# Optimization experiments

Measured on AMD Instinct MI355X. Metric: run time of the kernel, lower is better.

The kernel has to match this reference:

```python
import jax, jax.numpy as jnp
import numpy as np

N_NODES = 100000
N_EDGES = 1000000
IN_DIM = 128
HID1 = 64
HID2 = 64
OUT_DIM = 1
NUM_GRAPHS = 2048


def setup_inputs() -> dict:
    key = jax.random.key(0)
    ks = jax.random.split(key, 12)
    x = jax.random.normal(ks[0], (N_NODES, IN_DIM), dtype=jnp.float32)
    edge_index = jax.random.randint(ks[1], (2, N_EDGES), 0, N_NODES, dtype=jnp.int64)
    batch = jnp.sort(jax.random.randint(ks[2], (N_NODES,), 0, NUM_GRAPHS, dtype=jnp.int64))
    s1 = 1.0 / np.sqrt(IN_DIM)
    s2 = 1.0 / np.sqrt(HID1)
    s3 = 1.0 / np.sqrt(HID2)
    return {
        "x": x,
        "edge_index": edge_index,
        "batch": batch,
        "W1": jax.random.normal(ks[3], (IN_DIM, HID1), dtype=jnp.float32) * s1,
        "b1": jnp.zeros((HID1,), dtype=jnp.float32),
        "W2": jax.random.normal(ks[4], (HID1, HID2), dtype=jnp.float32) * s2,
        "b2": jnp.zeros((HID2,), dtype=jnp.float32),
        "attn_w": jax.random.normal(ks[5], (HID2, 1), dtype=jnp.float32) * s3,
        "attn_b": jnp.zeros((1,), dtype=jnp.float32),
        "mask_w": jax.random.normal(ks[6], (HID2, 1), dtype=jnp.float32) * s3,
        "mask_b": jnp.zeros((1,), dtype=jnp.float32),
        "out_w": jax.random.normal(ks[7], (HID2, OUT_DIM), dtype=jnp.float32) * s3,
        "out_b": jnp.zeros((OUT_DIM,), dtype=jnp.float32),
    }


def reference(x, edge_index, batch, W1, b1, W2, b2, attn_w, attn_b, mask_w, mask_b, out_w, out_b):
    n = x.shape[0]
    # GCNConv (PyG default): add self-loops, symmetric normalization
    loop = jnp.arange(n, dtype=edge_index.dtype)
    row = jnp.concatenate([edge_index[0], loop])  # source nodes
    col = jnp.concatenate([edge_index[1], loop])  # target nodes
    deg = jax.ops.segment_sum(jnp.ones_like(col, dtype=x.dtype), col, num_segments=n)
    dinv = jnp.where(deg > 0, jax.lax.rsqrt(jnp.maximum(deg, 1e-12)), 0.0)
    norm = dinv[row] * dinv[col]  # [E+N]

    def conv(h, W, b):
        h = h @ W                              # [N, out]
        m = h[row] * norm[:, None]             # gather + scale  [E+N, out]
        return jax.ops.segment_sum(m, col, num_segments=n) + b

    h = jax.nn.relu(conv(x, W1, b1))
    h = jax.nn.relu(conv(h, W2, b2))
    # AttentionPooling: (attn score * sigmoid mask)-weighted scatter-sum per graph
    scores = (h @ attn_w + attn_b) * jax.nn.sigmoid(h @ mask_w + mask_b)  # [N,1]
    pooled = jax.ops.segment_sum(h * scores, batch, num_segments=NUM_GRAPHS)  # [G, HID2]
    return pooled @ out_w + out_b
```

## Files before the change

### kernel.cpp

```cpp
#include <hip/hip_runtime.h>
#include <math.h>


#define NB 64
#define SEG 16
#define CAPS 80
#define SLOTS (SEG * CAPS)
#define BIN_BLOCKS 256

__global__ __launch_bounds__(256) void gemm_bin_kernel(
    const float* __restrict__ X, const float* __restrict__ W,
    float* __restrict__ P, int N, int K,
    const int* __restrict__ row, const int* __restrict__ col,
    int* __restrict__ bcnt, int* __restrict__ gbuf, int E,
    float* __restrict__ out, const float* __restrict__ out_b, int G) {
    __shared__ float Wl[32 * 64];
    __shared__ float xs[128 * 33];

    if (blockIdx.x < BIN_BLOCKS) {
        int seg = blockIdx.x & (SEG - 1);
        int t = blockIdx.x * 256 + threadIdx.x;
        if (t < G) out[t] = out_b[0];
        for (int e = t; e < E; e += BIN_BLOCKS * 256) {
            int c = col[e];
            int b = c >> 6;
            int pos = atomicAdd(&bcnt[(b * SEG + seg) * 16], 1);
            if (pos < CAPS) gbuf[b * SLOTS + seg * CAPS + pos] = row[e] | ((c & 63) << 17);
        }
        return;
    }

    const int tid = threadIdx.x;
    const int cg = tid & 3;
    const int ng = tid >> 2;
    const int node0 = (blockIdx.x - BIN_BLOCKS) * 128;

    float acc[2][16];
#pragma unroll
    for (int r = 0; r < 2; r++)
#pragma unroll
        for (int j = 0; j < 16; j++) acc[r][j] = 0.0f;

    for (int k0 = 0; k0 < K; k0 += 32) {
        const float4* Wg = (const float4*)(W + (size_t)k0 * 64);
#pragma unroll
        for (int f = tid; f < 512; f += 256) ((float4*)Wl)[f] = Wg[f];
        {
            int rrow = tid >> 1;
            int q0 = (tid & 1) * 16;
            int node = node0 + rrow;
            const float* Xr = X + (size_t)node * K + k0 + q0;
            float* xd = &xs[rrow * 33 + q0];
#pragma unroll
            for (int q = 0; q < 4; q++) {
                float4 v = make_float4(0.f, 0.f, 0.f, 0.f);
                if (node < N) v = *(const float4*)(Xr + 4 * q);
                xd[4 * q + 0] = v.x;
                xd[4 * q + 1] = v.y;
                xd[4 * q + 2] = v.z;
                xd[4 * q + 3] = v.w;
            }
        }
        __syncthreads();
#pragma unroll
        for (int kk = 0; kk < 32; kk++) {
            float xv0 = xs[(ng * 2 + 0) * 33 + kk];
            float xv1 = xs[(ng * 2 + 1) * 33 + kk];
            const float* wr = &Wl[kk * 64 + cg * 4];
            float4 w0 = *(const float4*)(wr + 0);
            float4 w1 = *(const float4*)(wr + 16);
            float4 w2 = *(const float4*)(wr + 32);
            float4 w3 = *(const float4*)(wr + 48);
#pragma unroll
            for (int r = 0; r < 2; r++) {
                float xv = r ? xv1 : xv0;
                acc[r][0]  = fmaf(xv, w0.x, acc[r][0]);
                acc[r][1]  = fmaf(xv, w0.y, acc[r][1]);
                acc[r][2]  = fmaf(xv, w0.z, acc[r][2]);
                acc[r][3]  = fmaf(xv, w0.w, acc[r][3]);
                acc[r][4]  = fmaf(xv, w1.x, acc[r][4]);
                acc[r][5]  = fmaf(xv, w1.y, acc[r][5]);
                acc[r][6]  = fmaf(xv, w1.z, acc[r][6]);
                acc[r][7]  = fmaf(xv, w1.w, acc[r][7]);
                acc[r][8]  = fmaf(xv, w2.x, acc[r][8]);
                acc[r][9]  = fmaf(xv, w2.y, acc[r][9]);
                acc[r][10] = fmaf(xv, w2.z, acc[r][10]);
                acc[r][11] = fmaf(xv, w2.w, acc[r][11]);
                acc[r][12] = fmaf(xv, w3.x, acc[r][12]);
                acc[r][13] = fmaf(xv, w3.y, acc[r][13]);
                acc[r][14] = fmaf(xv, w3.z, acc[r][14]);
                acc[r][15] = fmaf(xv, w3.w, acc[r][15]);
            }
        }
        __syncthreads();
    }

#pragma unroll
    for (int r = 0; r < 2; r++) {
        int node = node0 + ng * 2 + r;
        if (node < N) {
            float* dst = P + (size_t)node * 64 + cg * 4;
#pragma unroll
            for (int m = 0; m < 4; m++) {
                float4 v = make_float4(acc[r][4 * m + 0], acc[r][4 * m + 1],
                                       acc[r][4 * m + 2], acc[r][4 * m + 3]);
                *(float4*)(dst + 16 * m) = v;
            }
        }
    }
}

__global__ __launch_bounds__(256) void sort_kernel(
    const int* __restrict__ bcnt, const int* __restrict__ gbuf,
    int* __restrict__ csr, int* __restrict__ startcnt,
    float* __restrict__ dinv, int N) {
    __shared__ int scnt[SEG], segoff[SEG], s_tot;
    __shared__ int ebuf[SLOTS];
    __shared__ int lcnt[NB], lcur[NB];
    const int tid = threadIdx.x;
    const int b = blockIdx.x;
    const int base = b * SLOTS;

    if (tid < SEG) {
        int c = bcnt[(b * SEG + tid) * 16];
        scnt[tid] = c < CAPS ? c : CAPS;
    }
    if (tid < NB) lcnt[tid] = 0;
    __syncthreads();
    if (tid == 0) {
        int o = 0;
        for (int s = 0; s < SEG; s++) { segoff[s] = o; o += scnt[s]; }
        s_tot = o;
    }
    __syncthreads();
    for (int idx = tid; idx < SLOTS; idx += 256) {
        int seg = idx / CAPS;
        int j = idx - seg * CAPS;
        if (j < scnt[seg]) {
            int w = gbuf[base + idx];
            ebuf[segoff[seg] + j] = w;
            atomicAdd(&lcnt[(w >> 17) & 63], 1);
        }
    }
    __syncthreads();
    if (tid < NB) {
        int cntv = lcnt[tid];
        int rnd = (cntv + 3) & ~3;
        int val = rnd;
#pragma unroll
        for (int off = 1; off < 64; off <<= 1) {
            int n = __shfl_up(val, off, 64);
            if (tid >= off) val += n;
        }
        int st = val - rnd;
        lcur[tid] = st;
        int v = b * NB + tid;
        if (v < N) {
            dinv[v] = rsqrtf(1.0f + (float)cntv);
            int cc = cntv < 127 ? cntv : 127;
            startcnt[v] = ((base + st) << 7) | cc;
        }
    }
    __syncthreads();
    int tot = s_tot;
    for (int idx = tid; idx < tot; idx += 256) {
        int w = ebuf[idx];
        int vl = (w >> 17) & 63;
        int pp = atomicAdd(&lcur[vl], 1);
        csr[base + pp] = w & 131071;
    }
}

__global__ __launch_bounds__(256) void gather_gemm_kernel(
    const float* __restrict__ P, const int* __restrict__ csr,
    const int* __restrict__ startcnt, const float* __restrict__ dinv,
    const float* __restrict__ b1, const float* __restrict__ W2,
    float* __restrict__ Q, int N) {
    __shared__ float hs[64 * 65];
    __shared__ float Wl[64 * 64];
    const int tid = threadIdx.x;
    const int v0 = blockIdx.x * 64;
    const int vend = (v0 + 64 < N) ? v0 + 64 : N;
    const int p = tid & 15;
    const int p4 = p * 4;

    for (int f = tid; f < 1024; f += 256)
        ((float4*)Wl)[f] = ((const float4*)W2)[f];

    const float4 bb = ((const float4*)b1)[p];
    for (int v = v0 + (tid >> 4); v < vend; v += 16) {
        int pack = startcnt[v];
        int st = pack >> 7;
        int c = pack & 127;
        float dv = dinv[v];
        float4 a0 = *(const float4*)(P + (size_t)v * 64 + p4);
        float4 acc = make_float4(a0.x * dv, a0.y * dv, a0.z * dv, a0.w * dv);
        for (int i = 0; i < c; i += 8) {
            int4 ua = *(const int4*)(csr + st + i);
            int4 ub = *(const int4*)(csr + st + i + 4);
            float du0 = dinv[ua.x], du1 = dinv[ua.y], du2 = dinv[ua.z], du3 = dinv[ua.w];
            float du4 = dinv[ub.x], du5 = dinv[ub.y], du6 = dinv[ub.z], du7 = dinv[ub.w];
            float4 m0 = *(const float4*)(P + (size_t)ua.x * 64 + p4);
            float4 m1 = *(const float4*)(P + (size_t)ua.y * 64 + p4);
            float4 m2 = *(const float4*)(P + (size_t)ua.z * 64 + p4);
            float4 m3 = *(const float4*)(P + (size_t)ua.w * 64 + p4);
            float4 m4 = *(const float4*)(P + (size_t)ub.x * 64 + p4);
            float4 m5 = *(const float4*)(P + (size_t)ub.y * 64 + p4);
            float4 m6 = *(const float4*)(P + (size_t)ub.z * 64 + p4);
            float4 m7 = *(const float4*)(P + (size_t)ub.w * 64 + p4);
            acc.x = fmaf(m0.x, du0, acc.x); acc.y = fmaf(m0.y, du0, acc.y);
            acc.z = fmaf(m0.z, du0, acc.z); acc.w = fmaf(m0.w, du0, acc.w);
            if (i + 1 < c) { acc.x = fmaf(m1.x, du1, acc.x); acc.y = fmaf(m1.y, du1, acc.y);
                             acc.z = fmaf(m1.z, du1, acc.z); acc.w = fmaf(m1.w, du1, acc.w); }
            if (i + 2 < c) { acc.x = fmaf(m2.x, du2, acc.x); acc.y = fmaf(m2.y, du2, acc.y);
                             acc.z = fmaf(m2.z, du2, acc.z); acc.w = fmaf(m2.w, du2, acc.w); }
            if (i + 3 < c) { acc.x = fmaf(m3.x, du3, acc.x); acc.y = fmaf(m3.y, du3, acc.y);
                             acc.z = fmaf(m3.z, du3, acc.z); acc.w = fmaf(m3.w, du3, acc.w); }
            if (i + 4 < c) { acc.x = fmaf(m4.x, du4, acc.x); acc.y = fmaf(m4.y, du4, acc.y);
                             acc.z = fmaf(m4.z, du4, acc.z); acc.w = fmaf(m4.w, du4, acc.w); }
            if (i + 5 < c) { acc.x = fmaf(m5.x, du5, acc.x); acc.y = fmaf(m5.y, du5, acc.y);
                             acc.z = fmaf(m5.z, du5, acc.z); acc.w = fmaf(m5.w, du5, acc.w); }
            if (i + 6 < c) { acc.x = fmaf(m6.x, du6, acc.x); acc.y = fmaf(m6.y, du6, acc.y);
                             acc.z = fmaf(m6.z, du6, acc.z); acc.w = fmaf(m6.w, du6, acc.w); }
            if (i + 7 < c) { acc.x = fmaf(m7.x, du7, acc.x); acc.y = fmaf(m7.y, du7, acc.y);
                             acc.z = fmaf(m7.z, du7, acc.z); acc.w = fmaf(m7.w, du7, acc.w); }
        }
        float* hd = &hs[(v - v0) * 65 + p4];
        hd[0] = fmaxf(fmaf(acc.x, dv, bb.x), 0.f);
        hd[1] = fmaxf(fmaf(acc.y, dv, bb.y), 0.f);
        hd[2] = fmaxf(fmaf(acc.z, dv, bb.z), 0.f);
        hd[3] = fmaxf(fmaf(acc.w, dv, bb.w), 0.f);
    }
    __syncthreads();

    const int cg = tid & 3;
    const int n0 = tid >> 2;
    float acc[16];
#pragma unroll
    for (int j = 0; j < 16; j++) acc[j] = 0.0f;
    for (int kk = 0; kk < 64; kk++) {
        float xv = hs[n0 * 65 + kk];
        const float* wr = &Wl[kk * 64 + cg * 4];
        float4 w0 = *(const float4*)(wr + 0);
        float4 w1 = *(const float4*)(wr + 16);
        float4 w2 = *(const float4*)(wr + 32);
        float4 w3 = *(const float4*)(wr + 48);
        acc[0]  = fmaf(xv, w0.x, acc[0]);
        acc[1]  = fmaf(xv, w0.y, acc[1]);
        acc[2]  = fmaf(xv, w0.z, acc[2]);
        acc[3]  = fmaf(xv, w0.w, acc[3]);
        acc[4]  = fmaf(xv, w1.x, acc[4]);
        acc[5]  = fmaf(xv, w1.y, acc[5]);
        acc[6]  = fmaf(xv, w1.z, acc[6]);
        acc[7]  = fmaf(xv, w1.w, acc[7]);
        acc[8]  = fmaf(xv, w2.x, acc[8]);
        acc[9]  = fmaf(xv, w2.y, acc[9]);
        acc[10] = fmaf(xv, w2.z, acc[10]);
        acc[11] = fmaf(xv, w2.w, acc[11]);
        acc[12] = fmaf(xv, w3.x, acc[12]);
        acc[13] = fmaf(xv, w3.y, acc[13]);
        acc[14] = fmaf(xv, w3.z, acc[14]);
        acc[15] = fmaf(xv, w3.w, acc[15]);
    }
    int node = v0 + n0;
    if (node < N) {
        float d = dinv[node];
        float* dst = Q + (size_t)node * 64 + cg * 4;
        for (int m = 0; m < 4; m++) {
            float4 v = make_float4(acc[4 * m + 0] * d, acc[4 * m + 1] * d,
                                   acc[4 * m + 2] * d, acc[4 * m + 3] * d);
            *(float4*)(dst + 16 * m) = v;
        }
    }
}

#define GP_NODES 64
__global__ __launch_bounds__(256) void gather_pool_kernel(
    const float* __restrict__ Q, const int* __restrict__ csr,
    const int* __restrict__ startcnt, const float* __restrict__ dinv,
    const float* __restrict__ bias, const int* __restrict__ batch,
    const float* __restrict__ attn_w, const float* __restrict__ attn_b,
    const float* __restrict__ mask_w, const float* __restrict__ mask_b,
    const float* __restrict__ out_w, float* __restrict__ out, int N) {
    __shared__ float pacc[2048];
    __shared__ int s_gmin, s_span;
    const int tid = threadIdx.x;
    const int v0 = blockIdx.x * GP_NODES;
    const int vend = (v0 + GP_NODES < N) ? v0 + GP_NODES : N;
    if (tid == 0) {
        int gmin = batch[v0];
        s_gmin = gmin;
        s_span = batch[vend - 1] - gmin + 1;
    }
    __syncthreads();
    const int gmin = s_gmin, span = s_span;
    for (int i = tid; i < span; i += 256) pacc[i] = 0.f;
    __syncthreads();

    const int p = tid & 15;
    const int p4 = p * 4;
    const float4 wa = ((const float4*)attn_w)[p];
    const float4 wm = ((const float4*)mask_w)[p];
    const float4 wo = ((const float4*)out_w)[p];
    const float4 bb = ((const float4*)bias)[p];
    const float ab = attn_b[0], mb = mask_b[0];

    for (int v = v0 + (tid >> 4); v < vend; v += 16) {
        int pack = startcnt[v];
        int st = pack >> 7;
        int c = pack & 127;
        float dv = dinv[v];
        float4 acc = *(const float4*)(Q + (size_t)v * 64 + p4);
        for (int i = 0; i < c; i += 8) {
            int4 ua = *(const int4*)(csr + st + i);
            int4 ub = *(const int4*)(csr + st + i + 4);
            float4 m0 = *(const float4*)(Q + (size_t)ua.x * 64 + p4);
            float4 m1 = *(const float4*)(Q + (size_t)ua.y * 64 + p4);
            float4 m2 = *(const float4*)(Q + (size_t)ua.z * 64 + p4);
            float4 m3 = *(const float4*)(Q + (size_t)ua.w * 64 + p4);
            float4 m4 = *(const float4*)(Q + (size_t)ub.x * 64 + p4);
            float4 m5 = *(const float4*)(Q + (size_t)ub.y * 64 + p4);
            float4 m6 = *(const float4*)(Q + (size_t)ub.z * 64 + p4);
            float4 m7 = *(const float4*)(Q + (size_t)ub.w * 64 + p4);
            acc.x += m0.x; acc.y += m0.y; acc.z += m0.z; acc.w += m0.w;
            if (i + 1 < c) { acc.x += m1.x; acc.y += m1.y; acc.z += m1.z; acc.w += m1.w; }
            if (i + 2 < c) { acc.x += m2.x; acc.y += m2.y; acc.z += m2.z; acc.w += m2.w; }
            if (i + 3 < c) { acc.x += m3.x; acc.y += m3.y; acc.z += m3.z; acc.w += m3.w; }
            if (i + 4 < c) { acc.x += m4.x; acc.y += m4.y; acc.z += m4.z; acc.w += m4.w; }
            if (i + 5 < c) { acc.x += m5.x; acc.y += m5.y; acc.z += m5.z; acc.w += m5.w; }
            if (i + 6 < c) { acc.x += m6.x; acc.y += m6.y; acc.z += m6.z; acc.w += m6.w; }
            if (i + 7 < c) { acc.x += m7.x; acc.y += m7.y; acc.z += m7.z; acc.w += m7.w; }
        }
        float hx = fmaxf(fmaf(acc.x, dv, bb.x), 0.f);
        float hy = fmaxf(fmaf(acc.y, dv, bb.y), 0.f);
        float hz = fmaxf(fmaf(acc.z, dv, bb.z), 0.f);
        float hw = fmaxf(fmaf(acc.w, dv, bb.w), 0.f);
        float pa = hx * wa.x + hy * wa.y + hz * wa.z + hw * wa.w;
        float pm = hx * wm.x + hy * wm.y + hz * wm.z + hw * wm.w;
        float po = hx * wo.x + hy * wo.y + hz * wo.z + hw * wo.w;
#pragma unroll
        for (int off = 1; off < 16; off <<= 1) {
            pa += __shfl_xor(pa, off, 64);
            pm += __shfl_xor(pm, off, 64);
            po += __shfl_xor(po, off, 64);
        }
        if (p == 0) {
            float cc = (pa + ab) * (1.0f / (1.0f + expf(-(pm + mb)))) * po;
            atomicAdd(&pacc[batch[v] - gmin], cc);
        }
    }
    __syncthreads();
    for (int i = tid; i < span; i += 256) {
        float val = pacc[i];
        if (val != 0.f) atomicAdd(&out[gmin + i], val);
    }
}

extern "C" void kernel_launch(void* const* d_in, const int* in_sizes, int n_in,
                              void* d_out, int out_size, void* d_ws, size_t ws_size,
                              hipStream_t stream) {
    const float* x      = (const float*)d_in[0];
    const int*   edge   = (const int*)d_in[1];
    const int*   batch  = (const int*)d_in[2];
    const float* W1     = (const float*)d_in[3];
    const float* b1     = (const float*)d_in[4];
    const float* W2     = (const float*)d_in[5];
    const float* b2     = (const float*)d_in[6];
    const float* attn_w = (const float*)d_in[7];
    const float* attn_b = (const float*)d_in[8];
    const float* mask_w = (const float*)d_in[9];
    const float* mask_b = (const float*)d_in[10];
    const float* out_w  = (const float*)d_in[11];
    const float* out_b  = (const float*)d_in[12];
    float* out = (float*)d_out;

    const int N  = in_sizes[2];
    const int E  = in_sizes[1] / 2;
    const int K1 = in_sizes[0] / N;
    const int H  = in_sizes[4];
    const int G  = out_size;
    const int* row = edge;
    const int* col = edge + E;

    const int NBUCK = (N + NB - 1) / NB;

    char* ws = (char*)d_ws;
    auto align256 = [](size_t s) { return (s + 255) / 256 * 256; };
    int*   bcnt     = (int*)ws;   ws += align256((size_t)NBUCK * SEG * 16 * 4);
    int*   gbuf     = (int*)ws;   ws += align256((size_t)NBUCK * SLOTS * 4);
    int*   csr      = (int*)ws;   ws += align256((size_t)NBUCK * SLOTS * 4);
    int*   startcnt = (int*)ws;   ws += align256((size_t)N * 4);
    float* dinv     = (float*)ws; ws += align256((size_t)N * 4);
    float* P        = (float*)ws; ws += align256((size_t)N * H * 4);
    float* Q        = (float*)ws;

    const int gblocks = (N + 127) / 128;

    hipMemsetAsync(bcnt, 0, (size_t)NBUCK * SEG * 16 * 4, stream);
    hipMemsetAsync(csr, 0, (size_t)NBUCK * SLOTS * 4, stream);

    gemm_bin_kernel<<<BIN_BLOCKS + gblocks, 256, 0, stream>>>(
        x, W1, P, N, K1, row, col, bcnt, gbuf, E, out, out_b, G);

    sort_kernel<<<NBUCK, 256, 0, stream>>>(bcnt, gbuf, csr, startcnt, dinv, N);

    gather_gemm_kernel<<<NBUCK, 256, 0, stream>>>(
        P, csr, startcnt, dinv, b1, W2, Q, N);

    gather_pool_kernel<<<NBUCK, 256, 0, stream>>>(
        Q, csr, startcnt, dinv, b2, batch, attn_w, attn_b, mask_w, mask_b, out_w, out, N);
}
```

Baseline: 275.9 us.

## Move first GEMM from bin kernel into sort kernel, widen binning grid

Splits edge binning into a standalone kernel with four times as many blocks, and co-schedules the X@W1 GEMM blocks with the per-bucket sort blocks in one launch that shares a union shared-memory buffer. The aim is for the atomic-heavy binning to get full occupancy on its own, while the compute-bound GEMM overlaps the latency-bound sort. The cost is that the GEMM no longer overlaps the binning, and the wider grid raises atomic contention on the bucket counters.

```diff
diff --git a/kernel.cpp b/kernel.cpp
--- a/kernel.cpp
+++ b/kernel.cpp
@@ -6,34 +6,97 @@
 #define SEG 16
 #define CAPS 80
 #define SLOTS (SEG * CAPS)
-#define BIN_BLOCKS 256
-
-__global__ __launch_bounds__(256) void gemm_bin_kernel(
-    const float* __restrict__ X, const float* __restrict__ W,
-    float* __restrict__ P, int N, int K,
+#define BIN_BLOCKS 1024
+
+__global__ __launch_bounds__(256) void bin_kernel(
     const int* __restrict__ row, const int* __restrict__ col,
     int* __restrict__ bcnt, int* __restrict__ gbuf, int E,
     float* __restrict__ out, const float* __restrict__ out_b, int G) {
-    __shared__ float Wl[32 * 64];
-    __shared__ float xs[128 * 33];
-
-    if (blockIdx.x < BIN_BLOCKS) {
-        int seg = blockIdx.x & (SEG - 1);
-        int t = blockIdx.x * 256 + threadIdx.x;
-        if (t < G) out[t] = out_b[0];
-        for (int e = t; e < E; e += BIN_BLOCKS * 256) {
-            int c = col[e];
-            int b = c >> 6;
-            int pos = atomicAdd(&bcnt[(b * SEG + seg) * 16], 1);
-            if (pos < CAPS) gbuf[b * SLOTS + seg * CAPS + pos] = row[e] | ((c & 63) << 17);
+    int seg = blockIdx.x & (SEG - 1);
+    int t = blockIdx.x * 256 + threadIdx.x;
+    if (t < G) out[t] = out_b[0];
+    for (int e = t; e < E; e += BIN_BLOCKS * 256) {
+        int c = col[e];
+        int b = c >> 6;
+        int pos = atomicAdd(&bcnt[(b * SEG + seg) * 16], 1);
+        if (pos < CAPS) gbuf[b * SLOTS + seg * CAPS + pos] = row[e] | ((c & 63) << 17);
+    }
+}
+
+__global__ __launch_bounds__(256) void sort_gemm_kernel(
+    const int* __restrict__ bcnt, const int* __restrict__ gbuf,
+    int* __restrict__ csr, int* __restrict__ startcnt, float* __restrict__ dinv,
+    const float* __restrict__ X, const float* __restrict__ W,
+    float* __restrict__ P, int N, int K, int nbuck) {
+    __shared__ __align__(16) char smem[25088];
+    const int tid = threadIdx.x;
+
+    if ((int)blockIdx.x < nbuck) {
+        int* scnt   = (int*)smem;
+        int* segoff = scnt + SEG;
+        int* s_tot  = segoff + SEG;
+        int* lcnt   = s_tot + 1;
+        int* lcur   = lcnt + NB;
+        int* ebuf   = lcur + NB;
+        const int b = blockIdx.x;
+        const int base = b * SLOTS;
+
+        if (tid < SEG) {
+            int c = bcnt[(b * SEG + tid) * 16];
+            scnt[tid] = c < CAPS ? c : CAPS;
+        }
+        if (tid < NB) lcnt[tid] = 0;
+        __syncthreads();
+        if (tid == 0) {
+            int o = 0;
+            for (int s = 0; s < SEG; s++) { segoff[s] = o; o += scnt[s]; }
+            *s_tot = o;
+        }
+        __syncthreads();
+        for (int idx = tid; idx < SLOTS; idx += 256) {
+            int seg = idx / CAPS;
+            int j = idx - seg * CAPS;
+            if (j < scnt[seg]) {
+                int w = gbuf[base + idx];
+                ebuf[segoff[seg] + j] = w;
+                atomicAdd(&lcnt[(w >> 17) & 63], 1);
+            }
+        }
+        __syncthreads();
+        if (tid < NB) {
+            int cntv = lcnt[tid];
+            int rnd = (cntv + 3) & ~3;
+            int val = rnd;
+#pragma unroll
+            for (int off = 1; off < 64; off <<= 1) {
+                int n = __shfl_up(val, off, 64);
+                if (tid >= off) val += n;
+            }
+            int st = val - rnd;
+            lcur[tid] = st;
+            int v = b * NB + tid;
+            if (v < N) {
+                dinv[v] = rsqrtf(1.0f + (float)cntv);
+                int cc = cntv < 127 ? cntv : 127;
+                startcnt[v] = ((base + st) << 7) | cc;
+            }
+        }
+        __syncthreads();
+        int tot = *s_tot;
+        for (int idx = tid; idx < tot; idx += 256) {
+            int w = ebuf[idx];
+            int vl = (w >> 17) & 63;
+            int pp = atomicAdd(&lcur[vl], 1);
+            csr[base + pp] = w & 131071;
         }
         return;
     }
 
-    const int tid = threadIdx.x;
+    float* Wl = (float*)smem;
+    float* xs = Wl + 32 * 64;
     const int cg = tid & 3;
     const int ng = tid >> 2;
-    const int node0 = (blockIdx.x - BIN_BLOCKS) * 128;
+    const int node0 = (blockIdx.x - nbuck) * 128;
 
     float acc[2][16];
 #pragma unroll
@@ -107,67 +170,6 @@
                 *(float4*)(dst + 16 * m) = v;
             }
         }
-    }
-}
-
-__global__ __launch_bounds__(256) void sort_kernel(
-    const int* __restrict__ bcnt, const int* __restrict__ gbuf,
-    int* __restrict__ csr, int* __restrict__ startcnt,
-    float* __restrict__ dinv, int N) {
-    __shared__ int scnt[SEG], segoff[SEG], s_tot;
-    __shared__ int ebuf[SLOTS];
-    __shared__ int lcnt[NB], lcur[NB];
-    const int tid = threadIdx.x;
-    const int b = blockIdx.x;
-    const int base = b * SLOTS;
-
-    if (tid < SEG) {
-        int c = bcnt[(b * SEG + tid) * 16];
-        scnt[tid] = c < CAPS ? c : CAPS;
-    }
-    if (tid < NB) lcnt[tid] = 0;
-    __syncthreads();
-    if (tid == 0) {
-        int o = 0;
-        for (int s = 0; s < SEG; s++) { segoff[s] = o; o += scnt[s]; }
-        s_tot = o;
-    }
-    __syncthreads();
-    for (int idx = tid; idx < SLOTS; idx += 256) {
-        int seg = idx / CAPS;
-        int j = idx - seg * CAPS;
-        if (j < scnt[seg]) {
-            int w = gbuf[base + idx];
-            ebuf[segoff[seg] + j] = w;
-            atomicAdd(&lcnt[(w >> 17) & 63], 1);
-        }
-    }
-    __syncthreads();
-    if (tid < NB) {
-        int cntv = lcnt[tid];
-        int rnd = (cntv + 3) & ~3;
-        int val = rnd;
-#pragma unroll
-        for (int off = 1; off < 64; off <<= 1) {
-            int n = __shfl_up(val, off, 64);
-            if (tid >= off) val += n;
-        }
-        int st = val - rnd;
-        lcur[tid] = st;
-        int v = b * NB + tid;
-        if (v < N) {
-            dinv[v] = rsqrtf(1.0f + (float)cntv);
-            int cc = cntv < 127 ? cntv : 127;
-            startcnt[v] = ((base + st) << 7) | cc;
-        }
-    }
-    __syncthreads();
-    int tot = s_tot;
-    for (int idx = tid; idx < tot; idx += 256) {
-        int w = ebuf[idx];
-        int vl = (w >> 17) & 63;
-        int pp = atomicAdd(&lcur[vl], 1);
-        csr[base + pp] = w & 131071;
     }
 }
 
@@ -399,10 +401,10 @@
     hipMemsetAsync(bcnt, 0, (size_t)NBUCK * SEG * 16 * 4, stream);
     hipMemsetAsync(csr, 0, (size_t)NBUCK * SLOTS * 4, stream);
 
-    gemm_bin_kernel<<<BIN_BLOCKS + gblocks, 256, 0, stream>>>(
-        x, W1, P, N, K1, row, col, bcnt, gbuf, E, out, out_b, G);
-
-    sort_kernel<<<NBUCK, 256, 0, stream>>>(bcnt, gbuf, csr, startcnt, dinv, N);
+    bin_kernel<<<BIN_BLOCKS, 256, 0, stream>>>(row, col, bcnt, gbuf, E, out, out_b, G);
+
+    sort_gemm_kernel<<<NBUCK + gblocks, 256, 0, stream>>>(
+        bcnt, gbuf, csr, startcnt, dinv, x, W1, P, N, K1, NBUCK);
 
     gather_gemm_kernel<<<NBUCK, 256, 0, stream>>>(
         P, csr, startcnt, dinv, b1, W2, Q, N);
```

Measured after the change: 295.6 us. 1.07x slower.
